# Kernel tuning notes

Hardware: AMD Instinct MI355X
Metric: run time of the kernel (lower is better)

Reference implementation:

```python
import jax, jax.numpy as jnp
import numpy as np
import math

B, S, HID = 2, 2048, 1024
NH = 16
HD = HID // NH  # 64
CHUNK = 128  # min(128, S) from the module


def setup_inputs() -> dict:
    key = jax.random.key(0)
    ks = jax.random.split(key, 8)
    scale = 1.0 / math.sqrt(HID)
    return {
        "hidden_states": jax.random.normal(ks[0], (B, S, HID), jnp.float32),
        "attention_mask": jnp.zeros((B, S, S), jnp.float32),
        "Wq": jax.random.normal(ks[1], (HID, HID), jnp.float32) * scale,
        "bq": jnp.zeros((HID,), jnp.float32),
        "Wk": jax.random.normal(ks[2], (HID, HID), jnp.float32) * scale,
        "bk": jnp.zeros((HID,), jnp.float32),
        "Wv": jax.random.normal(ks[3], (HID, HID), jnp.float32) * scale,
        "bv": jnp.zeros((HID,), jnp.float32),
        "head_weights": jnp.ones((NH,), jnp.float32),
    }


def _split_heads(x):
    # [B,S,HID] -> [B,NH,S,HD]
    b, s, _ = x.shape
    return x.reshape(b, s, NH, HD).transpose(0, 2, 1, 3)


def reference(hidden_states, attention_mask, Wq, bq, Wk, bk, Wv, bv, head_weights):
    # nn.Linear: y = x @ W.T + b
    q = _split_heads(hidden_states @ Wq.T + bq)  # [B,NH,S,HD]
    k = _split_heads(hidden_states @ Wk.T + bk)
    v = _split_heads(hidden_states @ Wv.T + bv)

    scores = jnp.einsum("bhqd,bhkd->bhqk", q, k) / math.sqrt(HD)
    scores = scores + attention_mask[:, None, :, :]  # additive mask broadcast over heads
    probs = jax.nn.softmax(scores, axis=-1)
    # dropout p=0.0 -> identity; post-softmax head-weight scaling (head_pruning)
    probs = probs * head_weights[None, :, None, None]
    ctx = jnp.einsum("bhqk,bhkd->bhqd", probs, v)  # [B,NH,S,HD]
    context_layer = ctx.transpose(0, 2, 1, 3).reshape(B, S, HID)

    # module returns the probs of the LAST query chunk of the python loop
    last_start = ((S + CHUNK - 1) // CHUNK - 1) * CHUNK
    output_attention_probs = probs[:, :, last_start:S, :]  # [B,NH,128,S]
    return context_layer, output_attention_probs
```

## Files before the change

### kernel.cpp

```cpp
#include <hip/hip_runtime.h>

typedef unsigned short u16;
typedef __attribute__((ext_vector_type(8))) short bf16x8;
typedef __attribute__((ext_vector_type(4))) float f32x4;

#define B_   2
#define S_   2048
#define HID_ 1024
#define NH_  16
#define HD_  64
#define SCALE_ 0.125f

__device__ __forceinline__ u16 f2bf(float f) {
    union { float f; unsigned int i; } v; v.f = f;
    unsigned int r = v.i + 0x7fffu + ((v.i >> 16) & 1u);
    return (u16)(r >> 16);
}
__device__ __forceinline__ bf16x8 ld8(const u16* p) {
    return *reinterpret_cast<const bf16x8*>(p);
}
__device__ __forceinline__ unsigned cvtpk(float lo, float hi) {
    unsigned r;
    asm("v_cvt_pk_bf16_f32 %0, %1, %2" : "=v"(r) : "v"(lo), "v"(hi));
    return r;
}
__device__ __forceinline__ void gll16(const u16* g, const u16* l) {
    __builtin_amdgcn_global_load_lds(
        (const __attribute__((address_space(1))) unsigned int*)g,
        (__attribute__((address_space(3))) unsigned int*)l, 16, 0, 0);
}

__global__ __launch_bounds__(256) void conv_scan(
    const float* __restrict__ X, const float* __restrict__ W0,
    const float* __restrict__ W1, const float* __restrict__ W2,
    const unsigned* __restrict__ m,
    u16* __restrict__ Xb, u16* __restrict__ Wb, unsigned* __restrict__ flag)
{
    const int bx = blockIdx.x;
    if (bx < 3584) {
        const size_t s = (size_t)bx * 256 + threadIdx.x;
        const float* src; u16* dst; size_t off;
        if (s < 524288) { src = X; dst = Xb; off = s * 8; }
        else {
            const size_t t = s - 524288;
            const int w = (int)(t >> 17);
            off = (t & 131071) * 8;
            src = w == 0 ? W0 : w == 1 ? W1 : W2;
            dst = Wb + (size_t)w * 1048576;
        }
        f32x4 a = *(const f32x4*)(src + off);
        f32x4 b = *(const f32x4*)(src + off + 4);
        bf16x8 r;
        #pragma unroll
        for (int e = 0; e < 4; e++) { r[e] = (short)f2bf(a[e]); r[4 + e] = (short)f2bf(b[e]); }
        *(bf16x8*)(dst + off) = r;
    } else {
        const size_t i = ((size_t)(bx - 3584) * 256 + threadIdx.x) * 8;
        const uint4* p = (const uint4*)(m + i);
        uint4 a = p[0], b = p[1];
        const unsigned M = 0x7fffffffu;
        unsigned v = (a.x & M) | (a.y & M) | (a.z & M) | (a.w & M)
                   | (b.x & M) | (b.y & M) | (b.z & M) | (b.w & M);
        if (v) atomicOr(flag, 1u);
    }
}

#define BK_ 32

__global__ __launch_bounds__(256) void qkv_mfma(
    const u16* __restrict__ Xb, const u16* __restrict__ Wb,
    const float* __restrict__ bq, const float* __restrict__ bk,
    const float* __restrict__ bv,
    u16* __restrict__ Q, u16* __restrict__ K, u16* __restrict__ V)
{
    __shared__ __align__(16) u16 As[128 * BK_];
    __shared__ __align__(16) u16 Bs[128 * BK_];

    const int tid  = threadIdx.x;
    const int wave = tid >> 6;
    const int lane = tid & 63;
    const int l16  = lane & 15;
    const int quad = lane >> 4;
    const int wr   = wave >> 1, wc = wave & 1;

    const int id  = blockIdx.x + 32 * blockIdx.y;
    const int xcd = id & 7;
    const int kk  = id >> 3;
    const int i0  = (xcd * 4 + (kk & 3)) * 128;
    const int j0  = (kk >> 2) * 128;

    const int grow = (wave * 64 + lane) >> 2;
    const int gcol = (lane & 3) * 8;
    const u16* ldsA0 = As + wave * 512;
    const u16* ldsA1 = As + 2048 + wave * 512;
    const u16* ldsB0 = Bs + wave * 512;
    const u16* ldsB1 = Bs + 2048 + wave * 512;

    f32x4 acc[4][4] = {};

    for (int k0 = 0; k0 < HID_; k0 += BK_) {
        __syncthreads();
        gll16(Xb + (size_t)(i0 + grow) * HID_ + k0 + gcol, ldsA0);
        gll16(Xb + (size_t)(i0 + 64 + grow) * HID_ + k0 + gcol, ldsA1);
        gll16(Wb + (size_t)(j0 + grow) * HID_ + k0 + gcol, ldsB0);
        gll16(Wb + (size_t)(j0 + 64 + grow) * HID_ + k0 + gcol, ldsB1);
        __syncthreads();

        bf16x8 af[4], bfr[4];
        #pragma unroll
        for (int mt = 0; mt < 4; mt++)
            af[mt] = ld8(&As[(wr * 64 + mt * 16 + l16) * BK_ + quad * 8]);
        #pragma unroll
        for (int nt = 0; nt < 4; nt++)
            bfr[nt] = ld8(&Bs[(wc * 64 + nt * 16 + l16) * BK_ + quad * 8]);
        #pragma unroll
        for (int mt = 0; mt < 4; mt++)
            #pragma unroll
            for (int nt = 0; nt < 4; nt++)
                acc[mt][nt] = __builtin_amdgcn_mfma_f32_16x16x32_bf16(af[mt], bfr[nt], acc[mt][nt], 0, 0, 0);
    }

    const int which = j0 >> 10;
    const float* bias = which == 0 ? bq : which == 1 ? bk : bv;
    u16* Y            = which == 0 ? Q  : which == 1 ? K  : V;

    u16* bb = (wave < 2) ? (As + wave * 2048) : (Bs + (wave - 2) * 2048);

    #pragma unroll
    for (int p = 0; p < 2; p++) {
        __syncthreads();
        #pragma unroll
        for (int t2 = 0; t2 < 2; t2++) {
            const int nt = 2 * p + t2;
            const int j  = j0 + wc * 64 + nt * 16 + l16;
            const int jj = j & 1023;
            const float bv_ = bias[jj];
            #pragma unroll
            for (int mt = 0; mt < 4; mt++)
                #pragma unroll
                for (int r = 0; r < 4; r++) {
                    const int row = mt * 16 + quad * 4 + r;
                    const int col = t2 * 16 + l16;
                    const u16 val = f2bf(acc[mt][nt][r] + bv_);
                    if (which == 2)
                        bb[col * 64 + (row ^ ((col & 7) << 3))] = val;
                    else
                        bb[row * 32 + (col ^ ((row & 0xC) << 1))] = val;
                }
        }
        __syncthreads();
        #pragma unroll
        for (int k = 0; k < 4; k++) {
            const int c = lane + 64 * k;
            if (which == 2) {
                const int col  = c >> 3;
                const int row0 = (c & 7) * 8;
                bf16x8 v = ld8(&bb[col * 64 + (row0 ^ ((col & 7) << 3))]);
                const int j  = j0 + wc * 64 + p * 32 + col;
                const int jj = j & 1023;
                const int h = jj >> 6, d = jj & 63;
                const int i = i0 + wr * 64 + row0;
                const int b = i >> 11, s = i & (S_ - 1);
                *(bf16x8*)&Y[((size_t)(b * NH_ + h) * HD_ + d) * S_ + s] = v;
            } else {
                const int row  = c >> 2;
                const int col0 = (c & 3) * 8;
                bf16x8 v = ld8(&bb[row * 32 + (col0 ^ ((row & 0xC) << 1))]);
                const int j  = j0 + wc * 64 + p * 32 + col0;
                const int jj = j & 1023;
                const int h = jj >> 6, d = jj & 63;
                const int i = i0 + wr * 64 + row;
                const int b = i >> 11, s = i & (S_ - 1);
                *(bf16x8*)&Y[(((size_t)(b * NH_ + h) * S_ + s) * HD_) + d] = v;
            }
        }
    }
}

__global__ __launch_bounds__(256) void attn(
    const u16* __restrict__ Q, const u16* __restrict__ K, const u16* __restrict__ Vt,
    const float* __restrict__ mask, const float* __restrict__ hw,
    const unsigned* __restrict__ mflag,
    float* __restrict__ ctx, float* __restrict__ ml)
{
    __shared__ __align__(16) u16 Ks[2][64 * 64];
    __shared__ __align__(16) u16 Vs[2][64 * 64];
    __shared__ __align__(16) u16 Pl[4][16 * 64];

    const int usemask = (mflag[0] != 0);

    const int tid  = threadIdx.x;
    const int wave = tid >> 6;
    const int lane = tid & 63;
    const int l16  = lane & 15;
    const int quad = lane >> 4;
    const int x7   = l16 & 7;

    const int lin = blockIdx.x + 32 * (blockIdx.y + 16 * blockIdx.z);
    const int xcd = lin & 7, jj = lin >> 3;
    const int qb  = jj & 31;
    const int hb  = xcd * 4 + (jj >> 5);
    const int h   = hb & 15, b = hb >> 4;
    const int bh  = b * NH_ + h;

    const u16* Qh  = Q  + (size_t)bh * S_ * HD_;
    const u16* Kh  = K  + (size_t)bh * S_ * HD_;
    const u16* Vth = Vt + (size_t)bh * HD_ * S_;
    const float* Mb = mask + (size_t)b * S_ * S_;

    const int q0 = qb * 64 + wave * 16;

    bf16x8 qf0 = ld8(Qh + (size_t)(q0 + l16) * HD_ + quad * 8);
    bf16x8 qf1 = ld8(Qh + (size_t)(q0 + l16) * HD_ + 32 + quad * 8);

    f32x4 oacc[4] = {};
    float l_part[4] = {0.f, 0.f, 0.f, 0.f};

    const int srow = tid >> 3;
    const int sch  = tid & 7;
    const int ssw  = (sch ^ (srow & 7)) * 8;
    const int sL   = srow * 64 + ssw;

    {
        bf16x8 k0 = ld8(Kh + (size_t)srow * HD_ + sch * 8);
        bf16x8 k1 = ld8(Kh + (size_t)(srow + 32) * HD_ + sch * 8);
        bf16x8 v0 = ld8(Vth + (size_t)srow * S_ + sch * 8);
        bf16x8 v1 = ld8(Vth + (size_t)(srow + 32) * S_ + sch * 8);
        *(bf16x8*)&Ks[0][sL] = k0; *(bf16x8*)&Ks[0][sL + 2048] = k1;
        *(bf16x8*)&Vs[0][sL] = v0; *(bf16x8*)&Vs[0][sL + 2048] = v1;
    }
    __syncthreads();

    for (int t = 0; t < 32; ++t) {
        const int cur = t & 1;
        const int kt  = t * 64;
        const u16* Kb = Ks[cur];
        const u16* Vb = Vs[cur];

        bf16x8 kr0, kr1, vr0, vr1;
        if (t < 31) {
            const u16* Kg = Kh + (size_t)(kt + 64) * HD_;
            kr0 = ld8(Kg + (size_t)srow * HD_ + sch * 8);
            kr1 = ld8(Kg + (size_t)(srow + 32) * HD_ + sch * 8);
            vr0 = ld8(Vth + (size_t)srow * S_ + kt + 64 + sch * 8);
            vr1 = ld8(Vth + (size_t)(srow + 32) * S_ + kt + 64 + sch * 8);
        }

        f32x4 sacc[4] = {};
        __builtin_amdgcn_s_setprio(1);
        #pragma unroll
        for (int nb = 0; nb < 4; nb++) {
            const int base = (nb * 16 + l16) * 64;
            bf16x8 k0 = ld8(&Kb[base + ((quad ^ x7) * 8)]);
            bf16x8 k1 = ld8(&Kb[base + (((quad + 4) ^ x7) * 8)]);
            sacc[nb] = __builtin_amdgcn_mfma_f32_16x16x32_bf16(qf0, k0, sacc[nb], 0, 0, 0);
            sacc[nb] = __builtin_amdgcn_mfma_f32_16x16x32_bf16(qf1, k1, sacc[nb], 0, 0, 0);
        }
        __builtin_amdgcn_s_setprio(0);

        float p[4][4];
        if (usemask) {
            #pragma unroll
            for (int nb = 0; nb < 4; nb++)
                #pragma unroll
                for (int r = 0; r < 4; r++) {
                    const int qrow = q0 + quad * 4 + r;
                    const int key  = kt + nb * 16 + l16;
                    float s = sacc[nb][r] * SCALE_ + Mb[(size_t)qrow * S_ + key];
                    p[nb][r] = __expf(fminf(s, 80.f));
                    l_part[r] += p[nb][r];
                }
        } else {
            #pragma unroll
            for (int nb = 0; nb < 4; nb++)
                #pragma unroll
                for (int r = 0; r < 4; r++) {
                    p[nb][r] = __expf(fminf(sacc[nb][r] * SCALE_, 80.f));
                    l_part[r] += p[nb][r];
                }
        }

        {
            char* pbase = (char*)&Pl[wave][0];
            const int r0 = quad * 4;
            #pragma unroll
            for (int nb = 0; nb < 4; nb++) {
                const unsigned w01 = cvtpk(p[nb][0], p[nb][1]);
                const unsigned w23 = cvtpk(p[nb][2], p[nb][3]);
                const int c0 = nb * 32 + l16 * 2;
                *(u16*)(pbase + (r0 + 0) * 128 + (c0 ^ (((r0 + 0) & 7) << 4))) = (u16)w01;
                *(u16*)(pbase + (r0 + 1) * 128 + (c0 ^ (((r0 + 1) & 7) << 4))) = (u16)(w01 >> 16);
                *(u16*)(pbase + (r0 + 2) * 128 + (c0 ^ (((r0 + 2) & 7) << 4))) = (u16)w23;
                *(u16*)(pbase + (r0 + 3) * 128 + (c0 ^ (((r0 + 3) & 7) << 4))) = (u16)(w23 >> 16);
            }
        }

        __builtin_amdgcn_s_setprio(1);
        #pragma unroll
        for (int kb = 0; kb < 2; kb++) {
            const int c = kb * 4 + quad;
            bf16x8 pf = ld8(&Pl[wave][l16 * 64 + ((c ^ x7) * 8)]);
            #pragma unroll
            for (int db = 0; db < 4; db++) {
                bf16x8 vf = ld8(&Vb[(db * 16 + l16) * 64 + ((c ^ x7) * 8)]);
                oacc[db] = __builtin_amdgcn_mfma_f32_16x16x32_bf16(pf, vf, oacc[db], 0, 0, 0);
            }
        }
        __builtin_amdgcn_s_setprio(0);

        if (t < 31) {
            u16* Kd = Ks[cur ^ 1]; u16* Vd = Vs[cur ^ 1];
            *(bf16x8*)&Kd[sL] = kr0; *(bf16x8*)&Kd[sL + 2048] = kr1;
            *(bf16x8*)&Vd[sL] = vr0; *(bf16x8*)&Vd[sL + 2048] = vr1;
        }
        __syncthreads();
    }

    float l_i[4];
    #pragma unroll
    for (int r = 0; r < 4; r++) {
        float s = l_part[r];
        #pragma unroll
        for (int off = 1; off < 16; off <<= 1) s += __shfl_xor(s, off);
        l_i[r] = s;
    }

    const float hwf = hw[h];
    float invl[4];
    #pragma unroll
    for (int r = 0; r < 4; r++) invl[r] = hwf / l_i[r];

    #pragma unroll
    for (int db = 0; db < 4; db++)
        #pragma unroll
        for (int r = 0; r < 4; r++) {
            const int qrow = q0 + quad * 4 + r;
            ctx[((size_t)(b * S_ + qrow)) * HID_ + h * HD_ + db * 16 + l16] =
                oacc[db][r] * invl[r];
        }

    if (qb >= 30 && l16 == 0) {
        #pragma unroll
        for (int r = 0; r < 4; r++) {
            const int qrow = q0 + quad * 4 + r;
            ml[bh * 128 + (qrow - 1920)] = l_i[r];
        }
    }
}

__global__ __launch_bounds__(256) void probs_qk(
    const u16* __restrict__ Q, const u16* __restrict__ K,
    const float* __restrict__ mask, const float* __restrict__ hw,
    const unsigned* __restrict__ mflag, const float* __restrict__ ml,
    float* __restrict__ probs_out)
{
    const int usemask = (mflag[0] != 0);

    const int tid  = threadIdx.x;
    const int wave = tid >> 6;
    const int lane = tid & 63;
    const int l16  = lane & 15;
    const int quad = lane >> 4;

    const int rt = blockIdx.x & 1;
    const int ks = blockIdx.x >> 1;
    const int h  = blockIdx.y;
    const int b  = blockIdx.z;
    const int bh = b * NH_ + h;

    const u16* Qh = Q + (size_t)bh * S_ * HD_;
    const u16* Kh = K + (size_t)bh * S_ * HD_;
    const float* Mb = mask + (size_t)b * S_ * S_;

    const int q0   = 1920 + rt * 64 + wave * 16;
    const int qrow = q0 + l16;

    bf16x8 qf0 = ld8(Qh + (size_t)qrow * HD_ + quad * 8);
    bf16x8 qf1 = ld8(Qh + (size_t)qrow * HD_ + 32 + quad * 8);

    const float invl = hw[h] / ml[bh * 128 + (qrow - 1920)];
    float* Prow = probs_out + ((size_t)bh * 128 + (qrow - 1920)) * S_;
    const float* Mrow = Mb + (size_t)qrow * S_;

    for (int kt = ks * 256; kt < ks * 256 + 256; kt += 64) {
        f32x4 sacc[4] = {};
        #pragma unroll
        for (int nb = 0; nb < 4; nb++) {
            const u16* krow = Kh + (size_t)(kt + nb * 16 + l16) * HD_ + quad * 8;
            bf16x8 kA0 = ld8(krow);
            bf16x8 kA1 = ld8(krow + 32);
            sacc[nb] = __builtin_amdgcn_mfma_f32_16x16x32_bf16(kA0, qf0, sacc[nb], 0, 0, 0);
            sacc[nb] = __builtin_amdgcn_mfma_f32_16x16x32_bf16(kA1, qf1, sacc[nb], 0, 0, 0);
        }
        #pragma unroll
        for (int nb = 0; nb < 4; nb++) {
            const int kb0 = kt + nb * 16 + quad * 4;
            float4 v;
            if (usemask) {
                const float4 mv = *(const float4*)&Mrow[kb0];
                v.x = __expf(fminf(sacc[nb][0] * SCALE_ + mv.x, 80.f)) * invl;
                v.y = __expf(fminf(sacc[nb][1] * SCALE_ + mv.y, 80.f)) * invl;
                v.z = __expf(fminf(sacc[nb][2] * SCALE_ + mv.z, 80.f)) * invl;
                v.w = __expf(fminf(sacc[nb][3] * SCALE_ + mv.w, 80.f)) * invl;
            } else {
                v.x = __expf(fminf(sacc[nb][0] * SCALE_, 80.f)) * invl;
                v.y = __expf(fminf(sacc[nb][1] * SCALE_, 80.f)) * invl;
                v.z = __expf(fminf(sacc[nb][2] * SCALE_, 80.f)) * invl;
                v.w = __expf(fminf(sacc[nb][3] * SCALE_, 80.f)) * invl;
            }
            *(float4*)&Prow[kb0] = v;
        }
    }
}

extern "C" void kernel_launch(void* const* d_in, const int* in_sizes, int n_in,
                              void* d_out, int out_size, void* d_ws, size_t ws_size,
                              hipStream_t stream)
{
    const void* X = 0; const void* mask = 0; const void* hw = 0;
    const void* Wm[3] = {0, 0, 0}; const void* bm[3] = {0, 0, 0};
    int wi = 0, bi = 0;
    for (int i = 0; i < n_in; i++) {
        switch (in_sizes[i]) {
            case 4194304: X = d_in[i]; break;
            case 8388608: mask = d_in[i]; break;
            case 1048576: if (wi < 3) Wm[wi++] = d_in[i]; break;
            case 1024:    if (bi < 3) bm[bi++] = d_in[i]; break;
            case 16:      hw = d_in[i]; break;
            default: break;
        }
    }
    if (!X || !mask || wi != 3 || bi != 3 || !hw) {
        X = d_in[0]; mask = d_in[1];
        Wm[0] = d_in[2]; bm[0] = d_in[3];
        Wm[1] = d_in[4]; bm[1] = d_in[5];
        Wm[2] = d_in[6]; bm[2] = d_in[7];
        hw = d_in[8];
    }

    u16* Q  = (u16*)d_ws;
    u16* Kw = Q + 4194304ull;
    u16* Vw = Kw + 4194304ull;
    u16* Xb = Vw + 4194304ull;
    u16* Wb = Xb + 4194304ull;
    unsigned* flag = (unsigned*)(Wb + 3145728ull);
    float* ml = (float*)(flag + 64);

    float* ctx   = (float*)d_out;
    float* probs = ctx + (size_t)B_ * S_ * HID_;

    hipMemsetAsync(flag, 0, 4, stream);
    conv_scan<<<7680, 256, 0, stream>>>(
        (const float*)X, (const float*)Wm[0], (const float*)Wm[1], (const float*)Wm[2],
        (const unsigned*)mask, Xb, Wb, flag);

    qkv_mfma<<<dim3(32, 24), dim3(256), 0, stream>>>(
        Xb, Wb, (const float*)bm[0], (const float*)bm[1], (const float*)bm[2],
        Q, Kw, Vw);

    attn<<<dim3(32, 16, 2), dim3(256), 0, stream>>>(
        Q, Kw, Vw, (const float*)mask, (const float*)hw, flag, ctx, ml);

    probs_qk<<<dim3(16, 16, 2), dim3(256), 0, stream>>>(
        Q, Kw, (const float*)mask, (const float*)hw, flag, ml, probs);
}
```

Measured before the change: 238.8 us.

## Double QKV GEMM K-tile and transpose QK MFMA operands in attention

The QKV projection GEMM now stages a 64-wide K slice per iteration with a simple block mapping, which halves the number of barrier-synchronised load rounds. The previous XCD-aware tile swizzle is dropped. In the attention kernel the QK^T MFMA operands are swapped so each lane holds scores for one query row across four consecutive keys. This lets the mask be read as float4, P be written to LDS as 8-byte packed stores, and the row-sum reduction use two shuffles instead of four 16-lane reductions. The costs are larger LDS tiles in the GEMM and a shuffle redistribution of the inverse normaliser.

```diff
diff --git a/kernel.cpp b/kernel.cpp
--- a/kernel.cpp
+++ b/kernel.cpp
@@ -65,7 +65,7 @@
     }
 }
 
-#define BK_ 32
+#define BK_ 64
 
 __global__ __launch_bounds__(256) void qkv_mfma(
     const u16* __restrict__ Xb, const u16* __restrict__ Wb,
@@ -83,48 +83,46 @@
     const int quad = lane >> 4;
     const int wr   = wave >> 1, wc = wave & 1;
 
-    const int id  = blockIdx.x + 32 * blockIdx.y;
-    const int xcd = id & 7;
-    const int kk  = id >> 3;
-    const int i0  = (xcd * 4 + (kk & 3)) * 128;
-    const int j0  = (kk >> 2) * 128;
-
-    const int grow = (wave * 64 + lane) >> 2;
-    const int gcol = (lane & 3) * 8;
-    const u16* ldsA0 = As + wave * 512;
-    const u16* ldsA1 = As + 2048 + wave * 512;
-    const u16* ldsB0 = Bs + wave * 512;
-    const u16* ldsB1 = Bs + 2048 + wave * 512;
+    const int i0 = blockIdx.x * 128;
+    const int j0 = blockIdx.y * 128;
+
+    const int grow = lane >> 3;
+    const int gcol = (lane & 7) * 8;
 
     f32x4 acc[4][4] = {};
 
     for (int k0 = 0; k0 < HID_; k0 += BK_) {
         __syncthreads();
-        gll16(Xb + (size_t)(i0 + grow) * HID_ + k0 + gcol, ldsA0);
-        gll16(Xb + (size_t)(i0 + 64 + grow) * HID_ + k0 + gcol, ldsA1);
-        gll16(Wb + (size_t)(j0 + grow) * HID_ + k0 + gcol, ldsB0);
-        gll16(Wb + (size_t)(j0 + 64 + grow) * HID_ + k0 + gcol, ldsB1);
+        #pragma unroll
+        for (int g = 0; g < 4; g++) {
+            const int u = wave * 4 + g;
+            gll16(Xb + (size_t)(i0 + u * 8 + grow) * HID_ + k0 + gcol, As + u * 512);
+            gll16(Wb + (size_t)(j0 + u * 8 + grow) * HID_ + k0 + gcol, Bs + u * 512);
+        }
         __syncthreads();
 
-        bf16x8 af[4], bfr[4];
-        #pragma unroll
-        for (int mt = 0; mt < 4; mt++)
-            af[mt] = ld8(&As[(wr * 64 + mt * 16 + l16) * BK_ + quad * 8]);
-        #pragma unroll
-        for (int nt = 0; nt < 4; nt++)
-            bfr[nt] = ld8(&Bs[(wc * 64 + nt * 16 + l16) * BK_ + quad * 8]);
-        #pragma unroll
-        for (int mt = 0; mt < 4; mt++)
+        #pragma unroll
+        for (int kk = 0; kk < 2; kk++) {
+            bf16x8 af[4], bfr[4];
+            #pragma unroll
+            for (int mt = 0; mt < 4; mt++)
+                af[mt] = ld8(&As[(wr * 64 + mt * 16 + l16) * BK_ + kk * 32 + quad * 8]);
             #pragma unroll
             for (int nt = 0; nt < 4; nt++)
-                acc[mt][nt] = __builtin_amdgcn_mfma_f32_16x16x32_bf16(af[mt], bfr[nt], acc[mt][nt], 0, 0, 0);
+                bfr[nt] = ld8(&Bs[(wc * 64 + nt * 16 + l16) * BK_ + kk * 32 + quad * 8]);
+            #pragma unroll
+            for (int mt = 0; mt < 4; mt++)
+                #pragma unroll
+                for (int nt = 0; nt < 4; nt++)
+                    acc[mt][nt] = __builtin_amdgcn_mfma_f32_16x16x32_bf16(af[mt], bfr[nt], acc[mt][nt], 0, 0, 0);
+        }
     }
 
     const int which = j0 >> 10;
     const float* bias = which == 0 ? bq : which == 1 ? bk : bv;
     u16* Y            = which == 0 ? Q  : which == 1 ? K  : V;
 
-    u16* bb = (wave < 2) ? (As + wave * 2048) : (Bs + (wave - 2) * 2048);
+    u16* bb = As + wave * 2048;
 
     #pragma unroll
     for (int p = 0; p < 2; p++) {
@@ -214,7 +212,7 @@
     bf16x8 qf1 = ld8(Qh + (size_t)(q0 + l16) * HD_ + 32 + quad * 8);
 
     f32x4 oacc[4] = {};
-    float l_part[4] = {0.f, 0.f, 0.f, 0.f};
+    float l_part = 0.f;
 
     const int srow = tid >> 3;
     const int sch  = tid & 7;
@@ -253,45 +251,44 @@
             const int base = (nb * 16 + l16) * 64;
             bf16x8 k0 = ld8(&Kb[base + ((quad ^ x7) * 8)]);
             bf16x8 k1 = ld8(&Kb[base + (((quad + 4) ^ x7) * 8)]);
-            sacc[nb] = __builtin_amdgcn_mfma_f32_16x16x32_bf16(qf0, k0, sacc[nb], 0, 0, 0);
-            sacc[nb] = __builtin_amdgcn_mfma_f32_16x16x32_bf16(qf1, k1, sacc[nb], 0, 0, 0);
+            sacc[nb] = __builtin_amdgcn_mfma_f32_16x16x32_bf16(k0, qf0, sacc[nb], 0, 0, 0);
+            sacc[nb] = __builtin_amdgcn_mfma_f32_16x16x32_bf16(k1, qf1, sacc[nb], 0, 0, 0);
         }
         __builtin_amdgcn_s_setprio(0);
 
         float p[4][4];
         if (usemask) {
-            #pragma unroll
-            for (int nb = 0; nb < 4; nb++)
-                #pragma unroll
-                for (int r = 0; r < 4; r++) {
-                    const int qrow = q0 + quad * 4 + r;
-                    const int key  = kt + nb * 16 + l16;
-                    float s = sacc[nb][r] * SCALE_ + Mb[(size_t)qrow * S_ + key];
-                    p[nb][r] = __expf(fminf(s, 80.f));
-                    l_part[r] += p[nb][r];
-                }
+            const float* Mrow = Mb + (size_t)(q0 + l16) * S_ + kt;
+            #pragma unroll
+            for (int nb = 0; nb < 4; nb++) {
+                const float4 mv = *(const float4*)(Mrow + nb * 16 + quad * 4);
+                p[nb][0] = __expf(fminf(sacc[nb][0] * SCALE_ + mv.x, 80.f));
+                p[nb][1] = __expf(fminf(sacc[nb][1] * SCALE_ + mv.y, 80.f));
+                p[nb][2] = __expf(fminf(sacc[nb][2] * SCALE_ + mv.z, 80.f));
+                p[nb][3] = __expf(fminf(sacc[nb][3] * SCALE_ + mv.w, 80.f));
+                l_part += p[nb][0] + p[nb][1] + p[nb][2] + p[nb][3];
+            }
         } else {
             #pragma unroll
-            for (int nb = 0; nb < 4; nb++)
+            for (int nb = 0; nb < 4; nb++) {
                 #pragma unroll
                 for (int r = 0; r < 4; r++) {
                     p[nb][r] = __expf(fminf(sacc[nb][r] * SCALE_, 80.f));
-                    l_part[r] += p[nb][r];
+                    l_part += p[nb][r];
                 }
+            }
         }
 
         {
-            char* pbase = (char*)&Pl[wave][0];
-            const int r0 = quad * 4;
+            u16* prow = &Pl[wave][l16 * 64];
             #pragma unroll
             for (int nb = 0; nb < 4; nb++) {
-                const unsigned w01 = cvtpk(p[nb][0], p[nb][1]);
-                const unsigned w23 = cvtpk(p[nb][2], p[nb][3]);
-                const int c0 = nb * 32 + l16 * 2;
-                *(u16*)(pbase + (r0 + 0) * 128 + (c0 ^ (((r0 + 0) & 7) << 4))) = (u16)w01;
-                *(u16*)(pbase + (r0 + 1) * 128 + (c0 ^ (((r0 + 1) & 7) << 4))) = (u16)(w01 >> 16);
-                *(u16*)(pbase + (r0 + 2) * 128 + (c0 ^ (((r0 + 2) & 7) << 4))) = (u16)w23;
-                *(u16*)(pbase + (r0 + 3) * 128 + (c0 ^ (((r0 + 3) & 7) << 4))) = (u16)(w23 >> 16);
+                uint2 w;
+                w.x = cvtpk(p[nb][0], p[nb][1]);
+                w.y = cvtpk(p[nb][2], p[nb][3]);
+                const int ch  = 2 * nb + (quad >> 1);
+                const int off = ((ch ^ x7) << 3) + ((quad & 1) << 2);
+                *(uint2*)&prow[off] = w;
             }
         }
 
@@ -316,19 +313,16 @@
         __syncthreads();
     }
 
-    float l_i[4];
-    #pragma unroll
-    for (int r = 0; r < 4; r++) {
-        float s = l_part[r];
-        #pragma unroll
-        for (int off = 1; off < 16; off <<= 1) s += __shfl_xor(s, off);
-        l_i[r] = s;
-    }
-
-    const float hwf = hw[h];
+    float lsum = l_part;
+    lsum += __shfl_xor(lsum, 16);
+    lsum += __shfl_xor(lsum, 32);
+
+    const float hwf  = hw[h];
+    const float invq = hwf / lsum;
     float invl[4];
     #pragma unroll
-    for (int r = 0; r < 4; r++) invl[r] = hwf / l_i[r];
+    for (int r = 0; r < 4; r++)
+        invl[r] = __shfl(invq, (lane & 48) + quad * 4 + r);
 
     #pragma unroll
     for (int db = 0; db < 4; db++)
@@ -339,13 +333,8 @@
                 oacc[db][r] * invl[r];
         }
 
-    if (qb >= 30 && l16 == 0) {
-        #pragma unroll
-        for (int r = 0; r < 4; r++) {
-            const int qrow = q0 + quad * 4 + r;
-            ml[bh * 128 + (qrow - 1920)] = l_i[r];
-        }
-    }
+    if (qb >= 30 && quad == 0)
+        ml[bh * 128 + (q0 - 1920) + l16] = lsum;
 }
 
 __global__ __launch_bounds__(256) void probs_qk(
```

Result: no change. 241.2 us (+1.0%).
